# Kernel optimization log

Hardware: AMD Instinct MI355X
Metric: run time of the kernel (lower is better)

The kernel has to match this reference:

```python
import jax, jax.numpy as jnp
import numpy as np

BATCH = 32
IN_SHAPE = (64, 64)
OUT_SHAPE = (128, 128)


def setup_inputs() -> dict:
    key = jax.random.key(0)
    k1, k2 = jax.random.split(key)
    y = jax.random.normal(k1, (BATCH, *IN_SHAPE), dtype=jnp.float32)
    # normalized sample coordinates in [0,1), one per input dim
    xnew = jax.random.uniform(k2, (BATCH, *OUT_SHAPE, len(IN_SHAPE)), dtype=jnp.float32)
    return {"y": y, "xnew": xnew}


def reference(y, xnew):
    # y: [B, S1, S2]; xnew: [B, H, W, 2] with coords in [0,1)
    B = y.shape[0]
    s1, s2 = IN_SHAPE
    P = int(np.prod(OUT_SHAPE))
    x = xnew.reshape(B, P, 2)  # [B, P, 2]

    # FFT over spatial dims (dims 1..), as in torch.fft.fftn(..., dim=(1,2))
    F = jnp.fft.fftn(y, axes=(1, 2))  # [B, S1, S2] complex64

    # signed integer frequencies per dim (trigonometric interpolation)
    f1 = jnp.fft.fftfreq(s1).astype(jnp.float32) * s1  # [S1]
    f2 = jnp.fft.fftfreq(s2).astype(jnp.float32) * s2  # [S2]

    two_pi_i = 2j * jnp.pi
    # per-dim complex phase factors; separable NUFFT-type-2 evaluation
    E1 = jnp.exp(two_pi_i * x[..., 0:1] * f1)  # [B, P, S1]
    E2 = jnp.exp(two_pi_i * x[..., 1:2] * f2)  # [B, P, S2]

    # ynew[b,p] = (1/(S1*S2)) * sum_{k,m} F[b,k,m] E1[b,p,k] E2[b,p,m]
    ynew = jnp.einsum('bkm,bpk,bpm->bp', F, E1, E2) / (s1 * s2)
    ynew = jnp.real(ynew)
    return ynew.reshape(B, *OUT_SHAPE)
```

## Files before the change

kernel.cpp:

```cpp
#include <hip/hip_runtime.h>
#include <math.h>

typedef _Float16 f16x8 __attribute__((ext_vector_type(8)));
typedef _Float16 f16x2 __attribute__((ext_vector_type(2)));
typedef float    f32x4 __attribute__((ext_vector_type(4)));

union F16x8u { f16x8 v; f16x2 h[4]; };

__device__ __forceinline__ float cos1_hw(float x) { return __builtin_amdgcn_cosf(x); }
__device__ __forceinline__ float sin1_hw(float x) { return __builtin_amdgcn_sinf(x); }

__device__ __forceinline__ f16x2 pkrtz(float a, float b)
{
    return __builtin_bit_cast(f16x2, __builtin_amdgcn_cvt_pkrtz(a, b));
}


__global__ __launch_bounds__(1024, 4)
void fourier_fused(const float* __restrict__ y,
                   const float* __restrict__ xnew,
                   float* __restrict__ out)
{
    __shared__ _Float16 Yt [64 * 72];
    __shared__ _Float16 Trl[64 * 72];
    __shared__ _Float16 Til[64 * 72];
    __shared__ _Float16 FrL[64 * 72];
    __shared__ _Float16 FiL[64 * 72];
    __shared__ float2   XY[2048];
    __shared__ float2   tw[64];

    const int tid   = threadIdx.x;
    const int batch = blockIdx.x >> 3;
    const int sgrp  = blockIdx.x & 7;
    const int pbase = (batch << 14) + (sgrp << 11);

    ((float4*)XY)[tid] = ((const float4*)(xnew + ((size_t)pbase << 1)))[tid];
    {
        const float4 v = ((const float4*)(y + (batch << 12)))[tid];
        const int n1 = tid >> 4;
        const int n2 = (tid & 15) << 2;
        Yt[(n2 + 0) * 72 + n1] = (_Float16)v.x;
        Yt[(n2 + 1) * 72 + n1] = (_Float16)v.y;
        Yt[(n2 + 2) * 72 + n1] = (_Float16)v.z;
        Yt[(n2 + 3) * 72 + n1] = (_Float16)v.w;
    }
    if (tid < 64) {
        const float a = (float)tid * (1.0f / 64.0f);
        tw[tid] = make_float2(cos1_hw(a), sin1_hw(a));
    }
    __syncthreads();

    const int lane = tid & 63;
    const int wv   = tid >> 6;
    const int quad = lane >> 4;
    const int lrow = lane & 15;

    {
        const int rt   = wv >> 2;
        const int ct   = wv & 3;
        const int krow = (rt << 4) + lrow;
        f32x4 Tr = (f32x4){0.f, 0.f, 0.f, 0.f};
        f32x4 Ti = (f32x4){0.f, 0.f, 0.f, 0.f};
#pragma unroll
        for (int kt = 0; kt < 2; ++kt) {
            const int n1b = (kt << 5) + (quad << 3);
            F16x8u cf, sn;
#pragma unroll
            for (int jp = 0; jp < 4; ++jp) {
                const float2 wa = tw[(krow * (n1b + 2 * jp    )) & 63];
                const float2 wb = tw[(krow * (n1b + 2 * jp + 1)) & 63];
                cf.h[jp] = pkrtz(wa.x, wb.x);
                sn.h[jp] = pkrtz(-wa.y, -wb.y);
            }
            const f16x8 yf = *(const f16x8*)&Yt[((ct << 4) + lrow) * 72 + n1b];
            Tr = __builtin_amdgcn_mfma_f32_16x16x32_f16(cf.v, yf, Tr, 0, 0, 0);
            Ti = __builtin_amdgcn_mfma_f32_16x16x32_f16(sn.v, yf, Ti, 0, 0, 0);
        }
#pragma unroll
        for (int reg = 0; reg < 4; ++reg) {
            const int k = (rt << 4) + (quad << 2) + reg;
            Trl[k * 72 + (ct << 4) + lrow] = (_Float16)Tr[reg];
            Til[k * 72 + (ct << 4) + lrow] = (_Float16)Ti[reg];
        }
    }
    __syncthreads();

    {
        const int mt2 = wv >> 2;
        const int ct2 = wv & 3;
        const int mrow = (mt2 << 4) + lrow;
        f32x4 Fr = (f32x4){0.f, 0.f, 0.f, 0.f};
        f32x4 Fi = (f32x4){0.f, 0.f, 0.f, 0.f};
#pragma unroll
        for (int kt = 0; kt < 2; ++kt) {
            const int n2b = (kt << 5) + (quad << 3);
            F16x8u cf, sf, sn;
#pragma unroll
            for (int jp = 0; jp < 4; ++jp) {
                const float2 wa = tw[(mrow * (n2b + 2 * jp    )) & 63];
                const float2 wb = tw[(mrow * (n2b + 2 * jp + 1)) & 63];
                cf.h[jp] = pkrtz(wa.x, wb.x);
                sf.h[jp] = pkrtz(wa.y, wb.y);
                sn.h[jp] = pkrtz(-wa.y, -wb.y);
            }
            const f16x8 btr = *(const f16x8*)&Trl[((ct2 << 4) + lrow) * 72 + n2b];
            const f16x8 bti = *(const f16x8*)&Til[((ct2 << 4) + lrow) * 72 + n2b];
            Fr = __builtin_amdgcn_mfma_f32_16x16x32_f16(cf.v, btr, Fr, 0, 0, 0);
            Fr = __builtin_amdgcn_mfma_f32_16x16x32_f16(sf.v, bti, Fr, 0, 0, 0);
            Fi = __builtin_amdgcn_mfma_f32_16x16x32_f16(cf.v, bti, Fi, 0, 0, 0);
            Fi = __builtin_amdgcn_mfma_f32_16x16x32_f16(sn.v, btr, Fi, 0, 0, 0);
        }
#pragma unroll
        for (int reg = 0; reg < 4; ++reg) {
            const int m = (mt2 << 4) + (quad << 2) + reg;
            FrL[m * 72 + (ct2 << 4) + lrow] = (_Float16)Fr[reg];
            FiL[m * 72 + (ct2 << 4) + lrow] = (_Float16)Fi[reg];
        }
    }
    __syncthreads();

    f16x8 Ar[4][2], Ai[4][2];
#pragma unroll
    for (int nt = 0; nt < 4; ++nt)
#pragma unroll
        for (int kt = 0; kt < 2; ++kt) {
            const int off = ((nt << 4) + lrow) * 72 + (kt << 5) + (quad << 3);
            Ar[nt][kt] = *(const f16x8*)&FrL[off];
            Ai[nt][kt] = *(const f16x8*)&FiL[off];
        }

    const int mt0 = (wv >> 2) << 1;
#pragma unroll 1
    for (int it = 0; it < 8; ++it) {
        const int mt  = (it + mt0) & 7;
        const int lpt = ((mt >> 1) << 9) + (wv << 5) + ((mt & 1) << 4);
        const float2 xv = XY[lpt + lrow];

        const float cs1 = cos1_hw(xv.x);
        const float sn1 = sin1_hw(xv.x);
        const float cs1b = fmaf(cs1, cs1, -(sn1 * sn1));
        const float sn1b = 2.0f * cs1 * sn1;

        f32x4 Gr[4], Gi[4];
#pragma unroll
        for (int nt = 0; nt < 4; ++nt) {
            Gr[nt] = (f32x4){0.f, 0.f, 0.f, 0.f};
            Gi[nt] = (f32x4){0.f, 0.f, 0.f, 0.f};
        }

#pragma unroll
        for (int kt = 0; kt < 2; ++kt) {
            const float fb = (float)((quad << 3) - (kt ? 32 : 0));
            float th = xv.x * fb;
            th -= floorf(th);
            float er0 = cos1_hw(th);
            float ei0 = sin1_hw(th);
            float er1 = fmaf(-ei0, sn1, er0 * cs1);
            float ei1 = fmaf( er0, sn1, ei0 * cs1);

            F16x8u ur, ui, un;
#pragma unroll
            for (int jp = 0; jp < 4; ++jp) {
                ur.h[jp] = pkrtz(er0, er1);
                ui.h[jp] = pkrtz(ei0, ei1);
                un.h[jp] = pkrtz(-ei0, -ei1);
                if (jp < 3) {
                    const float e0 = fmaf(-ei0, sn1b, er0 * cs1b);
                    ei0 = fmaf(er0, sn1b, ei0 * cs1b);
                    er0 = e0;
                    const float e1 = fmaf(-ei1, sn1b, er1 * cs1b);
                    ei1 = fmaf(er1, sn1b, ei1 * cs1b);
                    er1 = e1;
                }
            }
#pragma unroll
            for (int nt = 0; nt < 4; ++nt) {
                Gr[nt] = __builtin_amdgcn_mfma_f32_16x16x32_f16(Ar[nt][kt], ur.v, Gr[nt], 0, 0, 0);
                Gr[nt] = __builtin_amdgcn_mfma_f32_16x16x32_f16(Ai[nt][kt], un.v, Gr[nt], 0, 0, 0);
                Gi[nt] = __builtin_amdgcn_mfma_f32_16x16x32_f16(Ar[nt][kt], ui.v, Gi[nt], 0, 0, 0);
                Gi[nt] = __builtin_amdgcn_mfma_f32_16x16x32_f16(Ai[nt][kt], ur.v, Gi[nt], 0, 0, 0);
            }
        }

        const float cs2 = cos1_hw(xv.y);
        const float sn2 = sin1_hw(xv.y);
        float t16 = xv.y * 16.0f;
        t16 -= floorf(t16);
        const float c16 = cos1_hw(t16);
        const float s16 = sin1_hw(t16);
        const float cm32 = fmaf(c16, c16, -(s16 * s16));
        const float sm32 = -2.0f * c16 * s16;

        float thA = xv.y * (float)(quad << 2);
        thA -= floorf(thA);
        const float erA = cos1_hw(thA);
        const float eiA = sin1_hw(thA);

        float br[4], bi[4];
        br[0] = erA;                            bi[0] = eiA;
        br[1] = fmaf(-eiA, s16, erA * c16);     bi[1] = fmaf(erA, s16, eiA * c16);
        br[2] = fmaf(-eiA, sm32, erA * cm32);   bi[2] = fmaf(erA, sm32, eiA * cm32);
        br[3] = fmaf(-bi[2], s16, br[2] * c16); bi[3] = fmaf(br[2], s16, bi[2] * c16);

        float red0 = 0.0f, red1 = 0.0f, red2 = 0.0f, red3 = 0.0f;
#pragma unroll
        for (int nt = 0; nt < 4; ++nt) {
            float er = br[nt];
            float ei = bi[nt];
            float acc = 0.0f;
#pragma unroll
            for (int reg = 0; reg < 4; ++reg) {
                acc = fmaf(Gr[nt][reg],  er, acc);
                acc = fmaf(Gi[nt][reg], -ei, acc);
                if (reg < 3) {
                    const float t2 = fmaf(-ei, sn2, er * cs2);
                    ei = fmaf(er, sn2, ei * cs2);
                    er = t2;
                }
            }
            if (nt == 0) red0 = acc;
            else if (nt == 1) red1 = acc;
            else if (nt == 2) red2 = acc;
            else red3 = acc;
        }
        float red = (red0 + red1) + (red2 + red3);
        red += __shfl_xor(red, 16, 64);
        red += __shfl_xor(red, 32, 64);
        if (lane < 16)
            out[pbase + lpt + lane] = red * (1.0f / 4096.0f);
    }
}

extern "C" void kernel_launch(void* const* d_in, const int* in_sizes, int n_in,
                              void* d_out, int out_size, void* d_ws, size_t ws_size,
                              hipStream_t stream)
{
    const float* y    = (const float*)d_in[0];
    const float* xnew = (const float*)d_in[1];
    float* out        = (float*)d_out;

    fourier_fused<<<256, 1024, 0, stream>>>(y, xnew, out);
}
```

Measured before the change: 77.10 us.

## Reorder MFMA accumulation per n-tile to shrink live accumulator registers

Builds all six dim-1 phase fragments first, then for each n-tile runs the eight MFMAs into one Gr/Gi pair and reduces it right away, instead of keeping all four Gr/Gi accumulators live across both k-steps. This cuts the accumulator registers held at once and may relieve register pressure under the 1024x4 launch bound. It also drops the per-wave staggered start index for the output-tile loop. The cost is longer dependent MFMA chains per tile and less interleaving of independent MFMAs, which can expose MFMA latency.

Result: no change. 77.05 us (-0.1%).

```diff
diff --git a/kernel.cpp b/kernel.cpp
--- a/kernel.cpp
+++ b/kernel.cpp
@@ -129,10 +129,8 @@
             Ai[nt][kt] = *(const f16x8*)&FiL[off];
         }
 
-    const int mt0 = (wv >> 2) << 1;
 #pragma unroll 1
-    for (int it = 0; it < 8; ++it) {
-        const int mt  = (it + mt0) & 7;
+    for (int mt = 0; mt < 8; ++mt) {
         const int lpt = ((mt >> 1) << 9) + (wv << 5) + ((mt & 1) << 4);
         const float2 xv = XY[lpt + lrow];
 
@@ -141,13 +139,7 @@
         const float cs1b = fmaf(cs1, cs1, -(sn1 * sn1));
         const float sn1b = 2.0f * cs1 * sn1;
 
-        f32x4 Gr[4], Gi[4];
-#pragma unroll
-        for (int nt = 0; nt < 4; ++nt) {
-            Gr[nt] = (f32x4){0.f, 0.f, 0.f, 0.f};
-            Gi[nt] = (f32x4){0.f, 0.f, 0.f, 0.f};
-        }
-
+        F16x8u ur0, ui0, un0, ur1, ui1, un1;
 #pragma unroll
         for (int kt = 0; kt < 2; ++kt) {
             const float fb = (float)((quad << 3) - (kt ? 32 : 0));
@@ -158,7 +150,9 @@
             float er1 = fmaf(-ei0, sn1, er0 * cs1);
             float ei1 = fmaf( er0, sn1, ei0 * cs1);
 
-            F16x8u ur, ui, un;
+            F16x8u& ur = kt ? ur1 : ur0;
+            F16x8u& ui = kt ? ui1 : ui0;
+            F16x8u& un = kt ? un1 : un0;
 #pragma unroll
             for (int jp = 0; jp < 4; ++jp) {
                 ur.h[jp] = pkrtz(er0, er1);
@@ -173,13 +167,6 @@
                     er1 = e1;
                 }
             }
-#pragma unroll
-            for (int nt = 0; nt < 4; ++nt) {
-                Gr[nt] = __builtin_amdgcn_mfma_f32_16x16x32_f16(Ar[nt][kt], ur.v, Gr[nt], 0, 0, 0);
-                Gr[nt] = __builtin_amdgcn_mfma_f32_16x16x32_f16(Ai[nt][kt], un.v, Gr[nt], 0, 0, 0);
-                Gi[nt] = __builtin_amdgcn_mfma_f32_16x16x32_f16(Ar[nt][kt], ui.v, Gi[nt], 0, 0, 0);
-                Gi[nt] = __builtin_amdgcn_mfma_f32_16x16x32_f16(Ai[nt][kt], ur.v, Gi[nt], 0, 0, 0);
-            }
         }
 
         const float cs2 = cos1_hw(xv.y);
@@ -205,13 +192,24 @@
         float red0 = 0.0f, red1 = 0.0f, red2 = 0.0f, red3 = 0.0f;
 #pragma unroll
         for (int nt = 0; nt < 4; ++nt) {
+            f32x4 Gr = (f32x4){0.f, 0.f, 0.f, 0.f};
+            f32x4 Gi = (f32x4){0.f, 0.f, 0.f, 0.f};
+            Gr = __builtin_amdgcn_mfma_f32_16x16x32_f16(Ar[nt][0], ur0.v, Gr, 0, 0, 0);
+            Gr = __builtin_amdgcn_mfma_f32_16x16x32_f16(Ai[nt][0], un0.v, Gr, 0, 0, 0);
+            Gr = __builtin_amdgcn_mfma_f32_16x16x32_f16(Ar[nt][1], ur1.v, Gr, 0, 0, 0);
+            Gr = __builtin_amdgcn_mfma_f32_16x16x32_f16(Ai[nt][1], un1.v, Gr, 0, 0, 0);
+            Gi = __builtin_amdgcn_mfma_f32_16x16x32_f16(Ar[nt][0], ui0.v, Gi, 0, 0, 0);
+            Gi = __builtin_amdgcn_mfma_f32_16x16x32_f16(Ai[nt][0], ur0.v, Gi, 0, 0, 0);
+            Gi = __builtin_amdgcn_mfma_f32_16x16x32_f16(Ar[nt][1], ui1.v, Gi, 0, 0, 0);
+            Gi = __builtin_amdgcn_mfma_f32_16x16x32_f16(Ai[nt][1], ur1.v, Gi, 0, 0, 0);
+
             float er = br[nt];
             float ei = bi[nt];
             float acc = 0.0f;
 #pragma unroll
             for (int reg = 0; reg < 4; ++reg) {
-                acc = fmaf(Gr[nt][reg],  er, acc);
-                acc = fmaf(Gi[nt][reg], -ei, acc);
+                acc = fmaf(Gr[reg],  er, acc);
+                acc = fmaf(Gi[reg], -ei, acc);
                 if (reg < 3) {
                     const float t2 = fmaf(-ei, sn2, er * cs2);
                     ei = fmaf(er, sn2, ei * cs2);
```
